# Kernel tuning notes

Measured on AMD Instinct MI355X. Metric: run time of the kernel, lower is better.

Reference implementation:

```python
import jax, jax.numpy as jnp
import numpy as np

N = 16          # num_transforms
BS = 128        # batch_size
D = 4096        # encoder dim
C, H, W = 3, 64, 64
TEMP = 0.5      # hyperparams.temperature
LAM_H = 1.0     # hyperparams.h
EPS = 1e-8      # torch CosineSimilarity eps


def setup_inputs() -> dict:
    key = jax.random.key(0)
    k1, k2, k3 = jax.random.split(key, 3)
    return {
        "pic_set": jax.random.normal(k1, (N, BS, C, H, W), dtype=jnp.float32),
        "dec_pics": jax.random.normal(k2, (N, BS, C, H, W), dtype=jnp.float32),
        "h": jax.random.normal(k3, (N, BS, D), dtype=jnp.float32),
    }


def _pos_neg_indices(n, bs):
    # Static (numpy) index construction replicating the boolean masks.
    # Positives of row i: all j != i with j % bs == i % bs (sorted, row-major),
    # Negatives of row i: all j with j % bs != i % bs (sorted).
    k = n * bs
    i = np.arange(k)
    cols = (i % bs)[:, None] + np.arange(n)[None, :] * bs          # (K, N)
    pos_idx = cols[cols != i[:, None]].reshape(k, n - 1)            # (K, N-1)
    jj = np.arange(k)
    neg_mask = (jj[None, :] % bs) != (i[:, None] % bs)              # (K, K)
    neg_idx = np.broadcast_to(jj, (k, k))[neg_mask].reshape(k, k - n)  # (K, K-N)
    return jnp.asarray(pos_idx), jnp.asarray(neg_idx)


def _nt_xent(h):
    n, bs, d = h.shape
    k = n * bs
    s = h.reshape(k, d)
    # CosineSimilarity(dim=2) with eps clamp on norms
    nrm = jnp.maximum(jnp.linalg.norm(s, axis=1), EPS)
    sn = s / nrm[:, None]
    simmat = (sn @ sn.T) / TEMP                                     # (K, K)
    pos_idx, neg_idx = _pos_neg_indices(n, bs)
    pos = jnp.take_along_axis(simmat, pos_idx, axis=1)              # (K, N-1)
    neg = jnp.take_along_axis(simmat, neg_idx, axis=1)              # (K, K-N)
    # CrossEntropyLoss(reduction='sum') with label 0 on logits
    # [pos_{i,m}, neg_i] == sum of logsumexp - pos; logsumexp over concat
    # factors as logaddexp(lse(neg_i), pos_{i,m}).
    neg_lse = jax.scipy.special.logsumexp(neg, axis=1)              # (K,)
    loss = jnp.sum(jnp.logaddexp(neg_lse[:, None], pos) - pos)
    kpos = k * (n - 1)
    return loss / kpos


def reference(pic_set, dec_pics, h):
    n, bs = pic_set.shape[0], pic_set.shape[1]
    loss_h = _nt_xent(h)
    # dec_pics[(i+1) % N] cyclic offset, then flat MSE (mean reduction)
    offset = (np.arange(n) + 1) % n
    p = pic_set.reshape(n, bs, -1)
    dshift = dec_pics.reshape(n, bs, -1)[offset]
    loss_pairs = jnp.mean((p - dshift) ** 2)
    return loss_pairs + LAM_H * loss_h
```

## Files before the change

kernel.cpp:

```cpp
#include <hip/hip_runtime.h>
#include <hip/hip_bf16.h>
#include <math.h>

#define N_T   16
#define BSZ   128
#define DDIM  4096
#define KROWS (N_T * BSZ)
#define CHW   (3 * 64 * 64)
#define S_PIC (BSZ * CHW)
#define T_MSE (N_T * S_PIC)
#define KPOS  (KROWS * (N_T - 1))

#define GEMM_BLOCKS 512
#define MSE_BLOCKS  3072

typedef short  bf16x8 __attribute__((ext_vector_type(8)));
typedef float  f32x4  __attribute__((ext_vector_type(4)));

__device__ __forceinline__ float waveReduceSum(float v) {
    for (int off = 32; off > 0; off >>= 1) v += __shfl_down(v, off, 64);
    return v;
}
__device__ __forceinline__ float waveReduceMax(float v) {
    for (int off = 32; off > 0; off >>= 1) v = fmaxf(v, __shfl_down(v, off, 64));
    return v;
}
__device__ __forceinline__ float blockReduceSum(float v) {
    __shared__ float s[8];
    int lane = threadIdx.x & 63, wid = threadIdx.x >> 6;
    v = waveReduceSum(v);
    if (lane == 0) s[wid] = v;
    __syncthreads();
    int nw = (blockDim.x + 63) >> 6;
    v = (threadIdx.x < nw) ? s[threadIdx.x] : 0.0f;
    if (wid == 0) v = waveReduceSum(v);
    return v;
}
__device__ __forceinline__ float blockReduceMax(float v) {
    __shared__ float s[8];
    int lane = threadIdx.x & 63, wid = threadIdx.x >> 6;
    v = waveReduceMax(v);
    if (lane == 0) s[wid] = v;
    __syncthreads();
    int nw = (blockDim.x + 63) >> 6;
    v = (threadIdx.x < nw) ? s[threadIdx.x] : -INFINITY;
    if (wid == 0) v = waveReduceMax(v);
    return v;
}

__device__ __forceinline__ void mse_block(const float* __restrict__ pic,
                                          const float* __restrict__ dec,
                                          float* __restrict__ acc,
                                          int n, int bx) {
    const size_t off = (size_t)n * S_PIC + (size_t)bx * 8192 + threadIdx.x * 4;
    const ptrdiff_t doff = (ptrdiff_t)(((n + 1) & (N_T - 1)) - n) * S_PIC;
    const float* p = pic + off;
    const float* d = pic + off;
    d = dec + off + doff;
    float s0 = 0.f, s1 = 0.f, s2 = 0.f, s3 = 0.f;
#pragma unroll
    for (int k = 0; k < 8; k++) {
        float4 a = *(const float4*)(p + k * 1024);
        float4 b = *(const float4*)(d + k * 1024);
        float dx = a.x - b.x, dy = a.y - b.y, dz = a.z - b.z, dw = a.w - b.w;
        s0 += dx * dx; s1 += dy * dy; s2 += dz * dz; s3 += dw * dw;
    }
    float sum = (s0 + s1) + (s2 + s3);
    sum = blockReduceSum(sum);
    if (threadIdx.x == 0) atomicAdd(acc, sum);
}

__global__ void norm_kernel(const float* __restrict__ h,
                            __hip_bfloat16* __restrict__ hb) {
    const int row = blockIdx.x;
    const float* r = h + (size_t)row * DDIM;
    float ss = 0.0f;
    for (int k = threadIdx.x * 8; k < DDIM; k += blockDim.x * 8) {
        float4 v0 = *(const float4*)(r + k);
        float4 v1 = *(const float4*)(r + k + 4);
        ss += v0.x * v0.x + v0.y * v0.y + v0.z * v0.z + v0.w * v0.w;
        ss += v1.x * v1.x + v1.y * v1.y + v1.z * v1.z + v1.w * v1.w;
    }
    ss = blockReduceSum(ss);
    __shared__ float scale_s;
    if (threadIdx.x == 0) scale_s = 1.0f / fmaxf(sqrtf(ss), 1e-8f);
    __syncthreads();
    const float sc = scale_s;
    __hip_bfloat16* ob = hb + (size_t)row * DDIM;
    for (int k = threadIdx.x * 8; k < DDIM; k += blockDim.x * 8) {
        float4 v0 = *(const float4*)(r + k);
        float4 v1 = *(const float4*)(r + k + 4);
        __hip_bfloat16 t[8];
        t[0] = __float2bfloat16(v0.x * sc); t[1] = __float2bfloat16(v0.y * sc);
        t[2] = __float2bfloat16(v0.z * sc); t[3] = __float2bfloat16(v0.w * sc);
        t[4] = __float2bfloat16(v1.x * sc); t[5] = __float2bfloat16(v1.y * sc);
        t[6] = __float2bfloat16(v1.z * sc); t[7] = __float2bfloat16(v1.w * sc);
        *(bf16x8*)(ob + k) = *(const bf16x8*)t;
    }
}

__global__ __launch_bounds__(256) void mega_kernel(const ushort* __restrict__ X,
                                                   float* __restrict__ Cpart,
                                                   const float* __restrict__ pic,
                                                   const float* __restrict__ dec,
                                                   float* __restrict__ acc) {
    __shared__ ushort As[128 * 32];
    __shared__ ushort Bs[128 * 32];
    const int bid = blockIdx.x;

    if (bid >= GEMM_BLOCKS) {
        const int t = bid - GEMM_BLOCKS;
        mse_block(pic, dec, acc, t & (N_T - 1), t >> 4);
        return;
    }

    const int kz = bid >> 8;
    const int bi = (bid >> 4) & 15, bj = bid & 15;
    const int tid  = threadIdx.x;
    const int wave = tid >> 6, lane = tid & 63;
    const int wm = wave >> 1, wn = wave & 1;
    const int quad = lane >> 4, l16 = lane & 15;

    f32x4 acc_r[4][4];
#pragma unroll
    for (int i = 0; i < 4; i++)
#pragma unroll
        for (int j = 0; j < 4; j++) acc_r[i][j] = (f32x4){0.f, 0.f, 0.f, 0.f};

    const int srow = lane >> 2;
    const int scol = (lane & 3) * 8;
    const ushort* Ag0 = X + (size_t)(bi * 128 + wave * 16       + srow) * DDIM + scol;
    const ushort* Ag1 = X + (size_t)(bi * 128 + (wave + 4) * 16 + srow) * DDIM + scol;
    const ushort* Bg0 = X + (size_t)(bj * 128 + wave * 16       + srow) * DDIM + scol;
    const ushort* Bg1 = X + (size_t)(bj * 128 + (wave + 4) * 16 + srow) * DDIM + scol;
    ushort* Al0 = As + wave * 512;
    ushort* Al1 = As + (wave + 4) * 512;
    ushort* Bl0 = Bs + wave * 512;
    ushort* Bl1 = Bs + (wave + 4) * 512;

    const int k0 = kz * (DDIM / 2), k1 = k0 + (DDIM / 2);
    for (int kk = k0; kk < k1; kk += 32) {
        __syncthreads();
        __builtin_amdgcn_global_load_lds(
            (const __attribute__((address_space(1))) unsigned int*)(Ag0 + kk),
            (__attribute__((address_space(3))) unsigned int*)Al0, 16, 0, 0);
        __builtin_amdgcn_global_load_lds(
            (const __attribute__((address_space(1))) unsigned int*)(Ag1 + kk),
            (__attribute__((address_space(3))) unsigned int*)Al1, 16, 0, 0);
        __builtin_amdgcn_global_load_lds(
            (const __attribute__((address_space(1))) unsigned int*)(Bg0 + kk),
            (__attribute__((address_space(3))) unsigned int*)Bl0, 16, 0, 0);
        __builtin_amdgcn_global_load_lds(
            (const __attribute__((address_space(1))) unsigned int*)(Bg1 + kk),
            (__attribute__((address_space(3))) unsigned int*)Bl1, 16, 0, 0);
        __syncthreads();

        bf16x8 a[4], b[4];
#pragma unroll
        for (int t = 0; t < 4; t++)
            a[t] = *(const bf16x8*)(As + (wm * 64 + t * 16 + l16) * 32 + quad * 8);
#pragma unroll
        for (int t = 0; t < 4; t++)
            b[t] = *(const bf16x8*)(Bs + (wn * 64 + t * 16 + l16) * 32 + quad * 8);
#pragma unroll
        for (int mt = 0; mt < 4; mt++)
#pragma unroll
            for (int nt = 0; nt < 4; nt++)
                acc_r[mt][nt] = __builtin_amdgcn_mfma_f32_16x16x32_bf16(
                    a[mt], b[nt], acc_r[mt][nt], 0, 0, 0);
    }

    float* Cp = Cpart + (size_t)kz * KROWS * KROWS;
#pragma unroll
    for (int mt = 0; mt < 4; mt++) {
#pragma unroll
        for (int r = 0; r < 4; r++) {
            const int row = bi * 128 + wm * 64 + mt * 16 + quad * 4 + r;
            float* o = Cp + (size_t)row * KROWS + bj * 128 + wn * 64 + l16;
#pragma unroll
            for (int nt = 0; nt < 4; nt++) o[nt * 16] = 2.0f * acc_r[mt][nt][r];
        }
    }
}

__global__ __launch_bounds__(256) void mse_kernel(const float* __restrict__ pic,
                                                  const float* __restrict__ dec,
                                                  float* __restrict__ acc) {
    mse_block(pic, dec, acc, blockIdx.y, blockIdx.x);
}

__global__ void lse_kernel(const float* __restrict__ Cpart, float* __restrict__ acc) {
    const int i = blockIdx.x;
    __shared__ float srow[KROWS];
    const float* r0 = Cpart + (size_t)i * KROWS;
    const float* r1 = r0 + (size_t)KROWS * KROWS;
    for (int j = threadIdx.x * 4; j < KROWS; j += blockDim.x * 4) {
        float4 a = *(const float4*)(r0 + j);
        float4 b = *(const float4*)(r1 + j);
        float4 s; s.x = a.x + b.x; s.y = a.y + b.y; s.z = a.z + b.z; s.w = a.w + b.w;
        *(float4*)(srow + j) = s;
    }
    __syncthreads();

    const int ires = i & (BSZ - 1);
    float m = -INFINITY;
    for (int j = threadIdx.x; j < KROWS; j += blockDim.x)
        if ((j & (BSZ - 1)) != ires) m = fmaxf(m, srow[j]);
    m = blockReduceMax(m);
    __shared__ float mS;
    if (threadIdx.x == 0) mS = m;
    __syncthreads();
    m = mS;
    float se = 0.0f;
    for (int j = threadIdx.x; j < KROWS; j += blockDim.x)
        if ((j & (BSZ - 1)) != ires) se += expf(srow[j] - m);
    se = blockReduceSum(se);

    if (threadIdx.x == 0) {
        const float neg_lse = m + logf(se);
        float loss = 0.0f;
#pragma unroll
        for (int t = 0; t < N_T; t++) {
            const int j = ires + t * BSZ;
            if (j == i) continue;
            const float x = neg_lse - srow[j];
            loss += (x > 0.0f) ? (x + log1pf(expf(-x))) : log1pf(expf(x));
        }
        atomicAdd(acc + 1, loss);
    }
}

__global__ void finalize_kernel(const float* __restrict__ acc, float* __restrict__ out) {
    if (threadIdx.x == 0 && blockIdx.x == 0)
        out[0] = acc[0] / (float)T_MSE + acc[1] / (float)KPOS;
}

extern "C" void kernel_launch(void* const* d_in, const int* in_sizes, int n_in,
                              void* d_out, int out_size, void* d_ws, size_t ws_size,
                              hipStream_t stream) {
    const float* pic = (const float*)d_in[0];
    float* dec = (float*)d_in[1];
    const float* h = (const float*)d_in[2];
    float* out = (float*)d_out;

    float* acc = (float*)d_ws;
    const size_t hbuf_bytes   = (size_t)KROWS * DDIM * sizeof(__hip_bfloat16);
    const size_t simmat_bytes = (size_t)2 * KROWS * KROWS * sizeof(float);

    hipMemsetAsync(d_ws, 0, 256, stream);

    if (ws_size >= 256 + hbuf_bytes + simmat_bytes) {
        __hip_bfloat16* hbuf = (__hip_bfloat16*)((char*)d_ws + 256);
        float* simmat = (float*)((char*)d_ws + 256 + hbuf_bytes);
        norm_kernel<<<KROWS, 256, 0, stream>>>(h, hbuf);
        mega_kernel<<<GEMM_BLOCKS + MSE_BLOCKS, 256, 0, stream>>>(
            (const ushort*)hbuf, simmat, pic, dec, acc);
        lse_kernel<<<KROWS, 256, 0, stream>>>(simmat, acc);
    } else {
        __hip_bfloat16* hbuf = (__hip_bfloat16*)dec;
        float* simmat = (float*)((char*)dec + hbuf_bytes);
        mse_kernel<<<dim3(MSE_BLOCKS / N_T, N_T), 256, 0, stream>>>(pic, dec, acc);
        norm_kernel<<<KROWS, 256, 0, stream>>>(h, hbuf);
        mega_kernel<<<GEMM_BLOCKS, 256, 0, stream>>>(
            (const ushort*)hbuf, simmat, pic, dec, acc);
        lse_kernel<<<KROWS, 256, 0, stream>>>(simmat, acc);
    }
    finalize_kernel<<<1, 64, 0, stream>>>(acc, out);
}
```

Measured before the change: 305.0 us.

## Fuse all stages into one persistent cooperative kernel with grid syncs

Replaces the memset plus norm, GEMM/MSE, LSE and finalize launches with a single cooperative kernel of 512 blocks. Stages are separated by grid.sync, and the final sum is taken deterministically from per-block partials instead of atomics. Within the GEMM/MSE stage, 256 blocks each do two GEMM tiles while the other 256 each handle 12 MSE chunks. This removes launch gaps and the memset, but adds grid-wide barriers, a fixed static split that can leave one half of the grid idle, and host occupancy queries on every call.

```diff
diff --git a/kernel.cpp b/kernel.cpp
--- a/kernel.cpp
+++ b/kernel.cpp
@@ -1,6 +1,9 @@
 #include <hip/hip_runtime.h>
 #include <hip/hip_bf16.h>
+#include <hip/hip_cooperative_groups.h>
 #include <math.h>
+
+namespace cg = cooperative_groups;
 
 #define N_T   16
 #define BSZ   128
@@ -11,8 +14,9 @@
 #define T_MSE (N_T * S_PIC)
 #define KPOS  (KROWS * (N_T - 1))
 
+#define COOP_BLOCKS 512
 #define GEMM_BLOCKS 512
-#define MSE_BLOCKS  3072
+#define MSE_JOBS    3072
 
 typedef short  bf16x8 __attribute__((ext_vector_type(8)));
 typedef float  f32x4  __attribute__((ext_vector_type(4)));
@@ -29,6 +33,7 @@
     __shared__ float s[8];
     int lane = threadIdx.x & 63, wid = threadIdx.x >> 6;
     v = waveReduceSum(v);
+    __syncthreads();
     if (lane == 0) s[wid] = v;
     __syncthreads();
     int nw = (blockDim.x + 63) >> 6;
@@ -40,6 +45,7 @@
     __shared__ float s[8];
     int lane = threadIdx.x & 63, wid = threadIdx.x >> 6;
     v = waveReduceMax(v);
+    __syncthreads();
     if (lane == 0) s[wid] = v;
     __syncthreads();
     int nw = (blockDim.x + 63) >> 6;
@@ -48,15 +54,13 @@
     return v;
 }
 
-__device__ __forceinline__ void mse_block(const float* __restrict__ pic,
-                                          const float* __restrict__ dec,
-                                          float* __restrict__ acc,
-                                          int n, int bx) {
+__device__ __forceinline__ float mse_chunk(const float* __restrict__ pic,
+                                           const float* __restrict__ dec,
+                                           int n, int bx) {
     const size_t off = (size_t)n * S_PIC + (size_t)bx * 8192 + threadIdx.x * 4;
     const ptrdiff_t doff = (ptrdiff_t)(((n + 1) & (N_T - 1)) - n) * S_PIC;
     const float* p = pic + off;
-    const float* d = pic + off;
-    d = dec + off + doff;
+    const float* d = dec + off + doff;
     float s0 = 0.f, s1 = 0.f, s2 = 0.f, s3 = 0.f;
 #pragma unroll
     for (int k = 0; k < 8; k++) {
@@ -65,17 +69,15 @@
         float dx = a.x - b.x, dy = a.y - b.y, dz = a.z - b.z, dw = a.w - b.w;
         s0 += dx * dx; s1 += dy * dy; s2 += dz * dz; s3 += dw * dw;
     }
-    float sum = (s0 + s1) + (s2 + s3);
-    sum = blockReduceSum(sum);
-    if (threadIdx.x == 0) atomicAdd(acc, sum);
-}
-
-__global__ void norm_kernel(const float* __restrict__ h,
-                            __hip_bfloat16* __restrict__ hb) {
-    const int row = blockIdx.x;
+    return (s0 + s1) + (s2 + s3);
+}
+
+__device__ __forceinline__ void norm_row(const float* __restrict__ h,
+                                         __hip_bfloat16* __restrict__ hb, int row) {
     const float* r = h + (size_t)row * DDIM;
     float ss = 0.0f;
-    for (int k = threadIdx.x * 8; k < DDIM; k += blockDim.x * 8) {
+#pragma unroll
+    for (int k = threadIdx.x * 8; k < DDIM; k += 2048) {
         float4 v0 = *(const float4*)(r + k);
         float4 v1 = *(const float4*)(r + k + 4);
         ss += v0.x * v0.x + v0.y * v0.y + v0.z * v0.z + v0.w * v0.w;
@@ -87,7 +89,8 @@
     __syncthreads();
     const float sc = scale_s;
     __hip_bfloat16* ob = hb + (size_t)row * DDIM;
-    for (int k = threadIdx.x * 8; k < DDIM; k += blockDim.x * 8) {
+#pragma unroll
+    for (int k = threadIdx.x * 8; k < DDIM; k += 2048) {
         float4 v0 = *(const float4*)(r + k);
         float4 v1 = *(const float4*)(r + k + 4);
         __hip_bfloat16 t[8];
@@ -99,23 +102,11 @@
     }
 }
 
-__global__ __launch_bounds__(256) void mega_kernel(const ushort* __restrict__ X,
-                                                   float* __restrict__ Cpart,
-                                                   const float* __restrict__ pic,
-                                                   const float* __restrict__ dec,
-                                                   float* __restrict__ acc) {
-    __shared__ ushort As[128 * 32];
-    __shared__ ushort Bs[128 * 32];
-    const int bid = blockIdx.x;
-
-    if (bid >= GEMM_BLOCKS) {
-        const int t = bid - GEMM_BLOCKS;
-        mse_block(pic, dec, acc, t & (N_T - 1), t >> 4);
-        return;
-    }
-
-    const int kz = bid >> 8;
-    const int bi = (bid >> 4) & 15, bj = bid & 15;
+__device__ __forceinline__ void gemm_tile(const ushort* __restrict__ X,
+                                          float* __restrict__ Cpart,
+                                          ushort* lds, int kz, int bi, int bj) {
+    ushort* As = lds;
+    ushort* Bs = lds + 4096;
     const int tid  = threadIdx.x;
     const int wave = tid >> 6, lane = tid & 63;
     const int wm = wave >> 1, wn = wave & 1;
@@ -181,20 +172,15 @@
             for (int nt = 0; nt < 4; nt++) o[nt * 16] = 2.0f * acc_r[mt][nt][r];
         }
     }
-}
-
-__global__ __launch_bounds__(256) void mse_kernel(const float* __restrict__ pic,
-                                                  const float* __restrict__ dec,
-                                                  float* __restrict__ acc) {
-    mse_block(pic, dec, acc, blockIdx.y, blockIdx.x);
-}
-
-__global__ void lse_kernel(const float* __restrict__ Cpart, float* __restrict__ acc) {
-    const int i = blockIdx.x;
-    __shared__ float srow[KROWS];
+    __syncthreads();
+}
+
+__device__ __forceinline__ float lse_row(const float* __restrict__ Cpart,
+                                         float* srow, int i) {
     const float* r0 = Cpart + (size_t)i * KROWS;
     const float* r1 = r0 + (size_t)KROWS * KROWS;
-    for (int j = threadIdx.x * 4; j < KROWS; j += blockDim.x * 4) {
+#pragma unroll
+    for (int j = threadIdx.x * 4; j < KROWS; j += 1024) {
         float4 a = *(const float4*)(r0 + j);
         float4 b = *(const float4*)(r1 + j);
         float4 s; s.x = a.x + b.x; s.y = a.y + b.y; s.z = a.z + b.z; s.w = a.w + b.w;
@@ -204,7 +190,8 @@
 
     const int ires = i & (BSZ - 1);
     float m = -INFINITY;
-    for (int j = threadIdx.x; j < KROWS; j += blockDim.x)
+#pragma unroll
+    for (int j = threadIdx.x; j < KROWS; j += 256)
         if ((j & (BSZ - 1)) != ires) m = fmaxf(m, srow[j]);
     m = blockReduceMax(m);
     __shared__ float mS;
@@ -212,13 +199,14 @@
     __syncthreads();
     m = mS;
     float se = 0.0f;
-    for (int j = threadIdx.x; j < KROWS; j += blockDim.x)
+#pragma unroll
+    for (int j = threadIdx.x; j < KROWS; j += 256)
         if ((j & (BSZ - 1)) != ires) se += expf(srow[j] - m);
     se = blockReduceSum(se);
 
+    float loss = 0.0f;
     if (threadIdx.x == 0) {
         const float neg_lse = m + logf(se);
-        float loss = 0.0f;
 #pragma unroll
         for (int t = 0; t < N_T; t++) {
             const int j = ires + t * BSZ;
@@ -226,10 +214,100 @@
             const float x = neg_lse - srow[j];
             loss += (x > 0.0f) ? (x + log1pf(expf(-x))) : log1pf(expf(x));
         }
-        atomicAdd(acc + 1, loss);
-    }
-}
-
+    }
+    __syncthreads();
+    return loss;
+}
+
+__global__ __launch_bounds__(256, 2) void coop_kernel(
+    const float* __restrict__ h, ushort* __restrict__ hbuf,
+    float* __restrict__ Cpart, const float* __restrict__ pic,
+    const float* __restrict__ dec, float* __restrict__ partials,
+    float* __restrict__ out) {
+    __shared__ ushort lds[128 * 32 * 2];
+    cg::grid_group grid = cg::this_grid();
+    const int bid = blockIdx.x;
+    const int tid = threadIdx.x;
+
+#pragma unroll
+    for (int r = 0; r < 4; r++) norm_row(h, (__hip_bfloat16*)hbuf, 4 * bid + r);
+    grid.sync();
+
+    float msesum = 0.0f;
+    if (bid < 256) {
+#pragma unroll
+        for (int j = 0; j < 2; j++) {
+            const int job = bid + 256 * j;
+            gemm_tile(hbuf, Cpart, lds, job >> 8, (job >> 4) & 15, job & 15);
+        }
+    } else {
+        const int b = bid - 256;
+#pragma unroll
+        for (int k2 = 0; k2 < 12; k2++) {
+            const int t = b + 256 * k2;
+            msesum += mse_chunk(pic, dec, t & (N_T - 1), t >> 4);
+        }
+    }
+    {
+        float s = blockReduceSum(msesum);
+        if (tid == 0) partials[bid] = s;
+    }
+    grid.sync();
+
+    {
+        float* srow = (float*)lds;
+        float l = 0.0f;
+#pragma unroll
+        for (int r = 0; r < 4; r++) l += lse_row(Cpart, srow, 4 * bid + r);
+        if (tid == 0) partials[COOP_BLOCKS + bid] = l;
+    }
+    grid.sync();
+
+    if (bid == 0) {
+        float v = 0.0f;
+#pragma unroll
+        for (int j = tid; j < 2 * COOP_BLOCKS; j += 256) {
+            float p = partials[j];
+            v += (j < COOP_BLOCKS) ? p * (1.0f / (float)T_MSE)
+                                   : p * (1.0f / (float)KPOS);
+        }
+        v = blockReduceSum(v);
+        if (tid == 0) out[0] = v;
+    }
+}
+
+__global__ __launch_bounds__(256) void mega_kernel(const ushort* __restrict__ X,
+                                                   float* __restrict__ Cpart,
+                                                   const float* __restrict__ pic,
+                                                   const float* __restrict__ dec,
+                                                   float* __restrict__ acc) {
+    __shared__ ushort lds[128 * 32 * 2];
+    const int bid = blockIdx.x;
+    if (bid >= GEMM_BLOCKS) {
+        const int t = bid - GEMM_BLOCKS;
+        float s = mse_chunk(pic, dec, t & (N_T - 1), t >> 4);
+        s = blockReduceSum(s);
+        if (threadIdx.x == 0) atomicAdd(acc, s);
+        return;
+    }
+    gemm_tile(X, Cpart, lds, bid >> 8, (bid >> 4) & 15, bid & 15);
+}
+__global__ __launch_bounds__(256) void mse_kernel(const float* __restrict__ pic,
+                                                  const float* __restrict__ dec,
+                                                  float* __restrict__ acc) {
+    float s = mse_chunk(pic, dec, blockIdx.y, blockIdx.x);
+    s = blockReduceSum(s);
+    if (threadIdx.x == 0) atomicAdd(acc, s);
+}
+__global__ void norm_kernel(const float* __restrict__ h,
+                            __hip_bfloat16* __restrict__ hb) {
+    norm_row(h, hb, blockIdx.x);
+}
+__global__ void lse_kernel(const float* __restrict__ Cpart, float* __restrict__ acc) {
+    __shared__ float srow[KROWS];
+    float l = lse_row(Cpart, srow, blockIdx.x);
+    if (threadIdx.x == 0) atomicAdd(acc + 1, l);
+}
 __global__ void finalize_kernel(const float* __restrict__ acc, float* __restrict__ out) {
     if (threadIdx.x == 0 && blockIdx.x == 0)
         out[0] = acc[0] / (float)T_MSE + acc[1] / (float)KPOS;
@@ -243,27 +321,47 @@
     const float* h = (const float*)d_in[2];
     float* out = (float*)d_out;
 
-    float* acc = (float*)d_ws;
+    const size_t part_bytes   = (size_t)2 * COOP_BLOCKS * sizeof(float);
     const size_t hbuf_bytes   = (size_t)KROWS * DDIM * sizeof(__hip_bfloat16);
     const size_t simmat_bytes = (size_t)2 * KROWS * KROWS * sizeof(float);
-
-    hipMemsetAsync(d_ws, 0, 256, stream);
-
-    if (ws_size >= 256 + hbuf_bytes + simmat_bytes) {
-        __hip_bfloat16* hbuf = (__hip_bfloat16*)((char*)d_ws + 256);
-        float* simmat = (float*)((char*)d_ws + 256 + hbuf_bytes);
-        norm_kernel<<<KROWS, 256, 0, stream>>>(h, hbuf);
-        mega_kernel<<<GEMM_BLOCKS + MSE_BLOCKS, 256, 0, stream>>>(
-            (const ushort*)hbuf, simmat, pic, dec, acc);
-        lse_kernel<<<KROWS, 256, 0, stream>>>(simmat, acc);
+    const size_t need = 256 + part_bytes + hbuf_bytes + simmat_bytes;
+
+    int dev = 0, nCU = 0, maxAct = 0;
+    hipGetDevice(&dev);
+    hipDeviceGetAttribute(&nCU, hipDeviceAttributeMultiprocessorCount, dev);
+    hipOccupancyMaxActiveBlocksPerMultiprocessor(&maxAct, (const void*)coop_kernel,
+                                                 256, 0);
+    const bool coop_ok = (ws_size >= need) && ((long)maxAct * nCU >= COOP_BLOCKS);
+
+    if (coop_ok) {
+        float*  partials = (float*)((char*)d_ws + 256);
+        ushort* hbuf     = (ushort*)((char*)d_ws + 256 + part_bytes);
+        float*  Cpart    = (float*)((char*)d_ws + 256 + part_bytes + hbuf_bytes);
+        void* args[] = {(void*)&h, (void*)&hbuf, (void*)&Cpart, (void*)&pic,
+                        (void*)&dec, (void*)&partials, (void*)&out};
+        hipLaunchCooperativeKernel((const void*)coop_kernel, dim3(COOP_BLOCKS),
+                                   dim3(256), args, 0, stream);
+    } else if (ws_size >= need) {
+        float* acc = (float*)d_ws;
+        float*  partials = (float*)((char*)d_ws + 256);
+        ushort* hbuf     = (ushort*)((char*)d_ws + 256 + part_bytes);
+        float*  Cpart    = (float*)((char*)d_ws + 256 + part_bytes + hbuf_bytes);
+        (void)partials;
+        hipMemsetAsync(d_ws, 0, 256, stream);
+        norm_kernel<<<KROWS, 256, 0, stream>>>(h, (__hip_bfloat16*)hbuf);
+        mega_kernel<<<GEMM_BLOCKS + MSE_JOBS, 256, 0, stream>>>(
+            hbuf, Cpart, pic, dec, acc);
+        lse_kernel<<<KROWS, 256, 0, stream>>>(Cpart, acc);
+        finalize_kernel<<<1, 64, 0, stream>>>(acc, out);
     } else {
-        __hip_bfloat16* hbuf = (__hip_bfloat16*)dec;
-        float* simmat = (float*)((char*)dec + hbuf_bytes);
-        mse_kernel<<<dim3(MSE_BLOCKS / N_T, N_T), 256, 0, stream>>>(pic, dec, acc);
-        norm_kernel<<<KROWS, 256, 0, stream>>>(h, hbuf);
-        mega_kernel<<<GEMM_BLOCKS, 256, 0, stream>>>(
-            (const ushort*)hbuf, simmat, pic, dec, acc);
-        lse_kernel<<<KROWS, 256, 0, stream>>>(simmat, acc);
-    }
-    finalize_kernel<<<1, 64, 0, stream>>>(acc, out);
-}
+        float* acc = (float*)d_ws;
+        ushort* hbuf = (ushort*)dec;
+        float* Cpart = (float*)((char*)dec + hbuf_bytes);
+        hipMemsetAsync(d_ws, 0, 256, stream);
+        mse_kernel<<<dim3(MSE_JOBS / N_T, N_T), 256, 0, stream>>>(pic, dec, acc);
+        norm_kernel<<<KROWS, 256, 0, stream>>>(h, (__hip_bfloat16*)hbuf);
+        mega_kernel<<<GEMM_BLOCKS, 256, 0, stream>>>(hbuf, Cpart, pic, dec, acc);
+        lse_kernel<<<KROWS, 256, 0, stream>>>(Cpart, acc);
+        finalize_kernel<<<1, 64, 0, stream>>>(acc, out);
+    }
+}
```

New measurement: 306.2 us. Within noise of the previous version (+0.4%).
